# Kernel optimization log

Measured on AMD Instinct MI355X. Metric: run time of the kernel, lower is better.

## Reference

```python
import jax, jax.numpy as jnp
import numpy as np

N_NODES = 207
N_EDGES = 1722
N_SLOTS = 288
RESOLUTION = 1
BATCH = 1024


def setup_inputs() -> dict:
    key = jax.random.key(0)
    ks = jax.random.split(key, 8)
    inputs = jax.random.normal(ks[0], (BATCH, 2, 12, N_NODES), dtype=jnp.float32)
    weight_react = jax.random.normal(ks[1], (N_SLOTS, N_EDGES), dtype=jnp.float32) / 10.0
    weight_diff = jax.random.normal(ks[2], (N_SLOTS, N_EDGES), dtype=jnp.float32) / 1000.0
    bias_reaction = jax.random.normal(ks[3], (N_SLOTS, N_NODES), dtype=jnp.float32) / 10.0
    bias_diffusion = jax.random.normal(ks[4], (N_SLOTS, N_NODES), dtype=jnp.float32) / 10.0
    weight_self_loop = jax.random.normal(ks[5], (N_SLOTS, N_NODES), dtype=jnp.float32) / 10.0
    ind = jax.random.randint(ks[6], (BATCH,), 0, N_SLOTS, dtype=jnp.int32)
    edge_index = jax.random.randint(ks[7], (2, N_EDGES), 0, N_NODES, dtype=jnp.int32)
    return {
        'inputs': inputs,
        'weight_react': weight_react,
        'weight_diff': weight_diff,
        'bias_reaction': bias_reaction,
        'bias_diffusion': bias_diffusion,
        'weight_self_loop': weight_self_loop,
        'ind': ind,
        'edge_index': edge_index,
    }


def _build_adjacency(edge_index, vals):
    """Symmetric dense adjacency per batch element.

    edge_index: [2, E] int; vals: [B, E] float.
    Returns A [B, N, N] with A[b, i, j] += v and A[b, j, i] += v (duplicates summed,
    matching torch.sparse_coo_tensor coalescing).
    """
    src = jnp.concatenate([edge_index[0], edge_index[1]])  # [2E]
    dst = jnp.concatenate([edge_index[1], edge_index[0]])  # [2E]
    v = jnp.concatenate([vals, vals], axis=1)              # [B, 2E]
    B = vals.shape[0]
    A = jnp.zeros((B, N_NODES, N_NODES), dtype=vals.dtype)
    return A.at[:, src, dst].add(v)


def reference(inputs, weight_react, weight_diff, bias_reaction, bias_diffusion,
              weight_self_loop, ind, edge_index):
    B = inputs.shape[0]
    # [B, d1, d2, N] -> [B, d1*d2, N] -> [B, N, L]
    x = inputs.reshape(B, -1, N_NODES).transpose(0, 2, 1)
    ii = ind // RESOLUTION  # time-of-day slot per sample, [B]

    A_r = _build_adjacency(edge_index, weight_react[ii])  # [B, N, N]
    A_d = _build_adjacency(edge_index, weight_diff[ii])   # [B, N, N]
    diag = jnp.arange(N_NODES)
    # torch sums dim 1 of [N, N] (column sums) and adds/subtracts diag of it
    d_r = A_r.sum(axis=1)  # [B, N]
    d_d = A_d.sum(axis=1)  # [B, N]
    R = A_r.at[:, diag, diag].add(d_r)   # diag(d) + A
    D = (-A_d).at[:, diag, diag].add(d_d)  # diag(d) - A

    # nconv: out[b, w, l] = sum_v x[b, v, l] * A[b, w, v]
    reaction = jnp.einsum('bvl,bwv->bwl', x, R) + bias_reaction[ii][:, :, None]
    diffusion = jnp.einsum('bvl,bwv->bwl', x, D) + bias_diffusion[ii][:, :, None]
    self_loop = weight_self_loop[ii][:, :, None] * x
    return jnp.tanh(reaction) + diffusion + x + self_loop  # [B, N, L]
```

## Files before the change

kernel.cpp:

```cpp
#include <hip/hip_runtime.h>

#define N_NODES 207
#define N_EDGES 1722
#define N_SLOTS 288
#define L_DIM 24
#define NPK 12
#define TOT_ENT (2 * N_EDGES)

typedef float f32x2 __attribute__((ext_vector_type(2)));
typedef __fp16 h16x2 __attribute__((ext_vector_type(2)));

__device__ __forceinline__ unsigned pkrtz(float a, float b) {
    h16x2 h = __builtin_amdgcn_cvt_pkrtz(a, b);
    return __builtin_bit_cast(unsigned, h);
}
__device__ __forceinline__ f32x2 h2f(unsigned u) {
    h16x2 h = __builtin_bit_cast(h16x2, u);
    f32x2 r; r.x = (float)h.x; r.y = (float)h.y;
    return r;
}
__device__ __forceinline__ void fma_lo(unsigned& acc, unsigned wt, unsigned x) {
    asm("v_pk_fma_f16 %0, %1, %2, %0 op_sel:[0,0,0] op_sel_hi:[0,1,1]"
        : "+v"(acc) : "v"(wt), "v"(x));
}
__device__ __forceinline__ void fma_hi(unsigned& acc, unsigned wt, unsigned x) {
    asm("v_pk_fma_f16 %0, %1, %2, %0 op_sel:[1,0,0] op_sel_hi:[1,1,1]"
        : "+v"(acc) : "v"(wt), "v"(x));
}
__device__ __forceinline__ void addw(unsigned& sw, unsigned wt) {
    asm("v_pk_add_f16 %0, %1, %0" : "+v"(sw) : "v"(wt));
}
__device__ __forceinline__ float fast_tanhf(float x) {
    float e2 = __expf(2.0f * x);
    return 1.0f - 2.0f * __builtin_amdgcn_rcpf(e2 + 1.0f);
}

__global__ __launch_bounds__(256) void build_csr_kernel(
    const int* __restrict__ edge_index,
    int* __restrict__ csr_off,
    unsigned int* __restrict__ entries,
    int* __restrict__ perm)
{
    __shared__ int cnt[N_NODES];
    __shared__ int cursor[N_NODES];
    __shared__ int wsum[4];
    __shared__ int dcur[64];
    const int tid  = threadIdx.x;
    const int lane = tid & 63;
    const int wid  = tid >> 6;

    if (tid < N_NODES) cnt[tid] = 0;
    if (tid < 64) dcur[tid] = 0;
    __syncthreads();

    for (int e = tid; e < N_EDGES; e += 256) {
        int i = edge_index[e];
        int j = edge_index[N_EDGES + e];
        atomicAdd(&cnt[i], 1);
        atomicAdd(&cnt[j], 1);
    }
    __syncthreads();

    const int deg = (tid < N_NODES) ? cnt[tid] : 0;
    int x = deg;
    #pragma unroll
    for (int s = 1; s < 64; s <<= 1) {
        int t = __shfl_up(x, s, 64);
        if (lane >= s) x += t;
    }
    if (lane == 63) wsum[wid] = x;
    int dcap = deg > 63 ? 63 : deg;
    if (tid < N_NODES) atomicAdd(&dcur[dcap], 1);
    __syncthreads();

    int base = 0;
    for (int i = 0; i < wid; ++i) base += wsum[i];
    const int excl = base + x - deg;
    if (tid < N_NODES) { csr_off[tid] = excl; cursor[tid] = excl; }
    if (tid == 255) {
        csr_off[N_NODES] = base + x;
        entries[TOT_ENT]     = 0u;
        entries[TOT_ENT + 1] = 0u;
    }

    if (tid < 64) {
        int h = dcur[63 - tid];
        int xs = h;
        #pragma unroll
        for (int s = 1; s < 64; s <<= 1) {
            int t = __shfl_up(xs, s, 64);
            if (lane >= s) xs += t;
        }
        __syncthreads();
        dcur[63 - tid] = xs - h;
    } else {
        __syncthreads();
    }
    __syncthreads();

    if (tid < N_NODES) {
        int p = atomicAdd(&dcur[dcap], 1);
        perm[p] = tid;
    }
    __syncthreads();

    for (int e = tid; e < N_EDGES; e += 256) {
        int i = edge_index[e];
        int j = edge_index[N_EDGES + e];
        int pi = atomicAdd(&cursor[i], 1);
        entries[pi] = (unsigned int)j | ((unsigned int)e << 16);
        int pj = atomicAdd(&cursor[j], 1);
        entries[pj] = (unsigned int)i | ((unsigned int)e << 16);
    }
}

__global__ __launch_bounds__(256, 4) void rdgcn_main_kernel(
    const float* __restrict__ x_in,
    const float* __restrict__ w_react,
    const float* __restrict__ w_diff,
    const float* __restrict__ b_react,
    const float* __restrict__ b_diff,
    const float* __restrict__ w_self,
    const int* __restrict__ ind,
    const int* __restrict__ csr_off,
    const unsigned int* __restrict__ entries,
    const int* __restrict__ perm,
    float* __restrict__ out)
{
    __shared__ unsigned x_sh[N_NODES * NPK];
    __shared__ unsigned wt_sh[N_EDGES];
    __shared__ unsigned ent_sh[TOT_ENT + 4];

    const int b   = blockIdx.x;
    const int tid = threadIdx.x;
    const int s   = ind[b];

    int w = 0, beg = 0, end = 0;
    float br = 0.f, bd = 0.f, wsl = 0.f;
    if (tid < N_NODES) {
        w   = perm[tid];
        beg = csr_off[w];
        end = csr_off[w + 1];
        br  = b_react[s * N_NODES + w];
        bd  = b_diff [s * N_NODES + w];
        wsl = w_self [s * N_NODES + w];
    }

    {
        const uint4* eg4 = reinterpret_cast<const uint4*>(entries);
        uint4* es4 = reinterpret_cast<uint4*>(ent_sh);
        for (int k = tid; k < TOT_ENT / 4; k += 256) es4[k] = eg4[k];
        if (tid == 0) { ent_sh[TOT_ENT] = 0u; ent_sh[TOT_ENT + 1] = 0u; }
    }
    const float* xg = x_in + (size_t)b * (L_DIM * N_NODES);
    if (tid < N_NODES) {
        float r[L_DIM];
        #pragma unroll
        for (int l = 0; l < L_DIM; ++l) r[l] = xg[l * N_NODES + tid];
        unsigned p[NPK];
        #pragma unroll
        for (int i = 0; i < NPK; ++i) p[i] = pkrtz(r[2*i], r[2*i+1]);
        uint4* dst = reinterpret_cast<uint4*>(&x_sh[tid * NPK]);
        dst[0] = make_uint4(p[0], p[1], p[2],  p[3]);
        dst[1] = make_uint4(p[4], p[5], p[6],  p[7]);
        dst[2] = make_uint4(p[8], p[9], p[10], p[11]);
    }
    {
        const float* wrg = w_react + (size_t)s * N_EDGES;
        const float* wdg = w_diff  + (size_t)s * N_EDGES;
        for (int e = tid; e < N_EDGES; e += 256)
            wt_sh[e] = pkrtz(wrg[e], wdg[e]);
    }
    __syncthreads();

    if (tid >= N_NODES) return;

    unsigned accr[NPK] = {0,0,0,0,0,0,0,0,0,0,0,0};
    unsigned accd[NPK] = {0,0,0,0,0,0,0,0,0,0,0,0};
    unsigned sw = 0;

    unsigned en = ent_sh[beg];
    for (int k = beg; k < end; ++k) {
        const unsigned en_nx = ent_sh[k + 1];
        const int nbr = (int)(en & 0xffffu);
        const int e   = (int)(en >> 16);
        const unsigned wt = wt_sh[e];
        const uint4* xr = reinterpret_cast<const uint4*>(&x_sh[nbr * NPK]);
        const uint4 qa = xr[0], qb = xr[1], qc = xr[2];
        en = en_nx;
        addw(sw, wt);
        fma_lo(accr[0],  wt, qa.x);   fma_hi(accd[0],  wt, qa.x);
        fma_lo(accr[1],  wt, qa.y);   fma_hi(accd[1],  wt, qa.y);
        fma_lo(accr[2],  wt, qa.z);   fma_hi(accd[2],  wt, qa.z);
        fma_lo(accr[3],  wt, qa.w);   fma_hi(accd[3],  wt, qa.w);
        fma_lo(accr[4],  wt, qb.x);   fma_hi(accd[4],  wt, qb.x);
        fma_lo(accr[5],  wt, qb.y);   fma_hi(accd[5],  wt, qb.y);
        fma_lo(accr[6],  wt, qb.z);   fma_hi(accd[6],  wt, qb.z);
        fma_lo(accr[7],  wt, qb.w);   fma_hi(accd[7],  wt, qb.w);
        fma_lo(accr[8],  wt, qc.x);   fma_hi(accd[8],  wt, qc.x);
        fma_lo(accr[9],  wt, qc.y);   fma_hi(accd[9],  wt, qc.y);
        fma_lo(accr[10], wt, qc.z);   fma_hi(accd[10], wt, qc.z);
        fma_lo(accr[11], wt, qc.w);   fma_hi(accd[11], wt, qc.w);
    }

    const f32x2 sw2 = h2f(sw);
    const float swr = sw2.x, swd = sw2.y;

    const uint4* xw = reinterpret_cast<const uint4*>(&x_sh[w * NPK]);
    const uint4 r0 = xw[0], r1 = xw[1], r2 = xw[2];
    const unsigned own[NPK] = { r0.x, r0.y, r0.z, r0.w,
                                r1.x, r1.y, r1.z, r1.w,
                                r2.x, r2.y, r2.z, r2.w };

    float o[L_DIM];
    #pragma unroll
    for (int i = 0; i < NPK; ++i) {
        const f32x2 xv = h2f(own[i]);
        const f32x2 ar = h2f(accr[i]);
        const f32x2 ad = h2f(accd[i]);
        {
            float re = fmaf(swr, xv.x,  ar.x) + br;
            float di = fmaf(swd, xv.x, -ad.x) + bd;
            o[2*i]   = fast_tanhf(re) + di + fmaf(xv.x, wsl, xv.x);
        }
        {
            float re = fmaf(swr, xv.y,  ar.y) + br;
            float di = fmaf(swd, xv.y, -ad.y) + bd;
            o[2*i+1] = fast_tanhf(re) + di + fmaf(xv.y, wsl, xv.y);
        }
    }
    float* op = out + (size_t)b * (N_NODES * L_DIM) + (size_t)w * L_DIM;
    reinterpret_cast<float4*>(op)[0] = make_float4(o[0],  o[1],  o[2],  o[3]);
    reinterpret_cast<float4*>(op)[1] = make_float4(o[4],  o[5],  o[6],  o[7]);
    reinterpret_cast<float4*>(op)[2] = make_float4(o[8],  o[9],  o[10], o[11]);
    reinterpret_cast<float4*>(op)[3] = make_float4(o[12], o[13], o[14], o[15]);
    reinterpret_cast<float4*>(op)[4] = make_float4(o[16], o[17], o[18], o[19]);
    reinterpret_cast<float4*>(op)[5] = make_float4(o[20], o[21], o[22], o[23]);
}

extern "C" void kernel_launch(void* const* d_in, const int* in_sizes, int n_in,
                              void* d_out, int out_size, void* d_ws, size_t ws_size,
                              hipStream_t stream) {
    const float* x_in     = (const float*)d_in[0];
    const float* w_react  = (const float*)d_in[1];
    const float* w_diff   = (const float*)d_in[2];
    const float* b_react  = (const float*)d_in[3];
    const float* b_diff   = (const float*)d_in[4];
    const float* w_self   = (const float*)d_in[5];
    const int*   ind      = (const int*)d_in[6];
    const int*   edge_idx = (const int*)d_in[7];
    float* out = (float*)d_out;

    char* wp = (char*)d_ws;
    int* csr_off = (int*)wp;
    wp += (((size_t)(N_NODES + 1) * sizeof(int)) + 255) & ~(size_t)255;
    unsigned int* entries = (unsigned int*)wp;
    wp += (((size_t)(TOT_ENT + 4) * sizeof(unsigned int)) + 255) & ~(size_t)255;
    int* perm = (int*)wp;

    build_csr_kernel<<<1, 256, 0, stream>>>(edge_idx, csr_off, entries, perm);

    const int B = in_sizes[6];
    rdgcn_main_kernel<<<B, 256, 0, stream>>>(x_in, w_react, w_diff,
                                             b_react, b_diff, w_self,
                                             ind, csr_off, entries, perm, out);
}
```

Before: 30.39 us.

## Fuse CSR construction into main kernel, rebuilding per block in shared memory

Drops the separate single-block CSR build kernel. Each batch block now rebuilds the edge CSR, degree-sorted permutation and offsets in shared memory, aliasing the x_sh buffer as scratch before it is filled. This removes one kernel launch and the serial dependency on a one-block kernel, plus the global round trip for the CSR tables. In exchange, every one of the 1024 blocks repeats the LDS atomics, scans and extra barriers, which lengthens each block's prologue.

```diff
diff --git a/kernel.cpp b/kernel.cpp
--- a/kernel.cpp
+++ b/kernel.cpp
@@ -35,86 +35,7 @@
     return 1.0f - 2.0f * __builtin_amdgcn_rcpf(e2 + 1.0f);
 }
 
-__global__ __launch_bounds__(256) void build_csr_kernel(
-    const int* __restrict__ edge_index,
-    int* __restrict__ csr_off,
-    unsigned int* __restrict__ entries,
-    int* __restrict__ perm)
-{
-    __shared__ int cnt[N_NODES];
-    __shared__ int cursor[N_NODES];
-    __shared__ int wsum[4];
-    __shared__ int dcur[64];
-    const int tid  = threadIdx.x;
-    const int lane = tid & 63;
-    const int wid  = tid >> 6;
-
-    if (tid < N_NODES) cnt[tid] = 0;
-    if (tid < 64) dcur[tid] = 0;
-    __syncthreads();
-
-    for (int e = tid; e < N_EDGES; e += 256) {
-        int i = edge_index[e];
-        int j = edge_index[N_EDGES + e];
-        atomicAdd(&cnt[i], 1);
-        atomicAdd(&cnt[j], 1);
-    }
-    __syncthreads();
-
-    const int deg = (tid < N_NODES) ? cnt[tid] : 0;
-    int x = deg;
-    #pragma unroll
-    for (int s = 1; s < 64; s <<= 1) {
-        int t = __shfl_up(x, s, 64);
-        if (lane >= s) x += t;
-    }
-    if (lane == 63) wsum[wid] = x;
-    int dcap = deg > 63 ? 63 : deg;
-    if (tid < N_NODES) atomicAdd(&dcur[dcap], 1);
-    __syncthreads();
-
-    int base = 0;
-    for (int i = 0; i < wid; ++i) base += wsum[i];
-    const int excl = base + x - deg;
-    if (tid < N_NODES) { csr_off[tid] = excl; cursor[tid] = excl; }
-    if (tid == 255) {
-        csr_off[N_NODES] = base + x;
-        entries[TOT_ENT]     = 0u;
-        entries[TOT_ENT + 1] = 0u;
-    }
-
-    if (tid < 64) {
-        int h = dcur[63 - tid];
-        int xs = h;
-        #pragma unroll
-        for (int s = 1; s < 64; s <<= 1) {
-            int t = __shfl_up(xs, s, 64);
-            if (lane >= s) xs += t;
-        }
-        __syncthreads();
-        dcur[63 - tid] = xs - h;
-    } else {
-        __syncthreads();
-    }
-    __syncthreads();
-
-    if (tid < N_NODES) {
-        int p = atomicAdd(&dcur[dcap], 1);
-        perm[p] = tid;
-    }
-    __syncthreads();
-
-    for (int e = tid; e < N_EDGES; e += 256) {
-        int i = edge_index[e];
-        int j = edge_index[N_EDGES + e];
-        int pi = atomicAdd(&cursor[i], 1);
-        entries[pi] = (unsigned int)j | ((unsigned int)e << 16);
-        int pj = atomicAdd(&cursor[j], 1);
-        entries[pj] = (unsigned int)i | ((unsigned int)e << 16);
-    }
-}
-
-__global__ __launch_bounds__(256, 4) void rdgcn_main_kernel(
+__global__ __launch_bounds__(256, 4) void rdgcn_fused_kernel(
     const float* __restrict__ x_in,
     const float* __restrict__ w_react,
     const float* __restrict__ w_diff,
@@ -122,35 +43,102 @@
     const float* __restrict__ b_diff,
     const float* __restrict__ w_self,
     const int* __restrict__ ind,
-    const int* __restrict__ csr_off,
-    const unsigned int* __restrict__ entries,
-    const int* __restrict__ perm,
+    const int* __restrict__ edge_index,
     float* __restrict__ out)
 {
     __shared__ unsigned x_sh[N_NODES * NPK];
     __shared__ unsigned wt_sh[N_EDGES];
     __shared__ unsigned ent_sh[TOT_ENT + 4];
 
-    const int b   = blockIdx.x;
-    const int tid = threadIdx.x;
-    const int s   = ind[b];
+    const int b    = blockIdx.x;
+    const int tid  = threadIdx.x;
+    const int lane = tid & 63;
+    const int wid  = tid >> 6;
+    const int s    = ind[b];
+
+    int* cnt_s  = (int*)x_sh;
+    int* cur_s  = cnt_s + 208;
+    int* off_s  = cur_s + 208;
+    int* perm_s = off_s + 209;
+    int* dcur_s = perm_s + 208;
+    int* wsum_s = dcur_s + 64;
+
+    if (tid < 208) cnt_s[tid] = 0;
+    if (tid < 64)  dcur_s[tid] = 0;
+    __syncthreads();
+
+    int ei[7], ej[7];
+    int ne = 0;
+    for (int e = tid; e < N_EDGES; e += 256) {
+        int i = edge_index[e];
+        int j = edge_index[N_EDGES + e];
+        ei[ne] = i; ej[ne] = j; ++ne;
+        atomicAdd(&cnt_s[i], 1);
+        atomicAdd(&cnt_s[j], 1);
+    }
+    __syncthreads();
+
+    const int deg = (tid < N_NODES) ? cnt_s[tid] : 0;
+    int xs = deg;
+    #pragma unroll
+    for (int sft = 1; sft < 64; sft <<= 1) {
+        int t = __shfl_up(xs, sft, 64);
+        if (lane >= sft) xs += t;
+    }
+    if (lane == 63) wsum_s[wid] = xs;
+    const int dcap = deg > 63 ? 63 : deg;
+    if (tid < N_NODES) atomicAdd(&dcur_s[dcap], 1);
+    __syncthreads();
+
+    int base = 0;
+    for (int i = 0; i < wid; ++i) base += wsum_s[i];
+    const int excl = base + xs - deg;
+    if (tid < N_NODES) { off_s[tid] = excl; cur_s[tid] = excl; }
+    if (tid == 255)    off_s[N_NODES] = base + xs;
+
+    if (tid < 64) {
+        int h = dcur_s[63 - tid];
+        int ys = h;
+        #pragma unroll
+        for (int sft = 1; sft < 64; sft <<= 1) {
+            int t = __shfl_up(ys, sft, 64);
+            if (lane >= sft) ys += t;
+        }
+        __syncthreads();
+        dcur_s[63 - tid] = ys - h;
+    } else {
+        __syncthreads();
+    }
+    __syncthreads();
+
+    if (tid < N_NODES) {
+        int p = atomicAdd(&dcur_s[dcap], 1);
+        perm_s[p] = tid;
+    }
+    for (int q = 0; q < ne; ++q) {
+        const int i = ei[q], j = ej[q];
+        const int e = tid + q * 256;
+        int pi = atomicAdd(&cur_s[i], 1);
+        ent_sh[pi] = (unsigned)j | ((unsigned)e << 16);
+        int pj = atomicAdd(&cur_s[j], 1);
+        ent_sh[pj] = (unsigned)i | ((unsigned)e << 16);
+    }
+    if (tid == 0) { ent_sh[TOT_ENT] = 0u; ent_sh[TOT_ENT + 1] = 0u; }
+    __syncthreads();
 
     int w = 0, beg = 0, end = 0;
+    if (tid < N_NODES) {
+        w   = perm_s[tid];
+        beg = off_s[w];
+        end = off_s[w + 1];
+    }
+    __syncthreads();
+
     float br = 0.f, bd = 0.f, wsl = 0.f;
     if (tid < N_NODES) {
-        w   = perm[tid];
-        beg = csr_off[w];
-        end = csr_off[w + 1];
         br  = b_react[s * N_NODES + w];
         bd  = b_diff [s * N_NODES + w];
         wsl = w_self [s * N_NODES + w];
-    }
-
-    {
-        const uint4* eg4 = reinterpret_cast<const uint4*>(entries);
-        uint4* es4 = reinterpret_cast<uint4*>(ent_sh);
-        for (int k = tid; k < TOT_ENT / 4; k += 256) es4[k] = eg4[k];
-        if (tid == 0) { ent_sh[TOT_ENT] = 0u; ent_sh[TOT_ENT + 1] = 0u; }
     }
     const float* xg = x_in + (size_t)b * (L_DIM * N_NODES);
     if (tid < N_NODES) {
@@ -251,17 +239,8 @@
     const int*   edge_idx = (const int*)d_in[7];
     float* out = (float*)d_out;
 
-    char* wp = (char*)d_ws;
-    int* csr_off = (int*)wp;
-    wp += (((size_t)(N_NODES + 1) * sizeof(int)) + 255) & ~(size_t)255;
-    unsigned int* entries = (unsigned int*)wp;
-    wp += (((size_t)(TOT_ENT + 4) * sizeof(unsigned int)) + 255) & ~(size_t)255;
-    int* perm = (int*)wp;
-
-    build_csr_kernel<<<1, 256, 0, stream>>>(edge_idx, csr_off, entries, perm);
-
     const int B = in_sizes[6];
-    rdgcn_main_kernel<<<B, 256, 0, stream>>>(x_in, w_react, w_diff,
-                                             b_react, b_diff, w_self,
-                                             ind, csr_off, entries, perm, out);
-}
+    rdgcn_fused_kernel<<<B, 256, 0, stream>>>(x_in, w_react, w_diff,
+                                              b_react, b_diff, w_self,
+                                              ind, edge_idx, out);
+}
```

New measurement: 27.04 us. -11.0%, faster.
